# Kernel tuning notes

Measured on AMD Instinct MI355X. Metric: run time of the kernel, lower is better.

## Reference

```python
import jax, jax.numpy as jnp
import numpy as np

N = 4096
IN, HID, OUT = 512, 512, 512
EMB, MHID = 64, 128
GRID_SIZE, SPLINE_ORDER = 5, 3
D_B = GRID_SIZE + SPLINE_ORDER + 1      # 9
SPLINE_DIM = GRID_SIZE + SPLINE_ORDER   # 8


def make_grid():
    h = (1.0 - (-1.0)) / GRID_SIZE
    return jnp.arange(-SPLINE_ORDER, GRID_SIZE + SPLINE_ORDER + 1, dtype=jnp.float32) * h - 1.0


def b_splines(x, grid):
    # x: (N, in) -> (N, in, SPLINE_DIM); Cox-de Boor recursion, epsilon-stabilized
    xg = x[..., None]
    bases = ((xg >= grid[:-1]) & (xg < grid[1:])).astype(x.dtype)
    eps = 1e-08
    for k in range(1, SPLINE_ORDER + 1):
        dp = grid[k:-1] - grid[:-(k + 1)]
        dn = grid[k + 1:] - grid[1:-k]
        bases = (xg - grid[:-(k + 1)]) / (dp + eps) * bases[..., :-1] \
              + (grid[k + 1:] - xg) / (dn + eps) * bases[..., 1:]
    return bases


def _xavier(k, shape):
    fan_out, fan_in = shape
    std = (2.0 / (fan_in + fan_out)) ** 0.5
    return std * jax.random.normal(k, shape, jnp.float32)


def setup_inputs() -> dict:
    key = jax.random.key(0)
    ks = jax.random.split(key, 7)
    x = 2.0 * jax.random.uniform(ks[0], (N, IN), jnp.float32) - 1.0
    inp = {"x": x}
    dims = [(IN, HID), (HID, OUT)]
    for i, (fi, fo) in enumerate(dims):
        kk = jax.random.split(ks[i + 1], 3)
        inp[f"emb{i}"] = _xavier(kk[0], (fi * fo, EMB))   # layout: (out, in) flattened, out outer
        inp[f"w1_{i}"] = _xavier(kk[1], (MHID, EMB))
        inp[f"b1_{i}"] = jnp.zeros((MHID,), jnp.float32)
        inp[f"w2_{i}"] = _xavier(kk[2], (D_B, MHID))
        inp[f"b2_{i}"] = jnp.zeros((D_B,), jnp.float32)
    return inp


def _kan_layer(h, emb, w1, b1, w2, b2, in_f, out_f, grid):
    basis = b_splines(h, grid)                              # (N, in, SPLINE_DIM)
    w = (emb @ w1.T + b1) @ w2.T + b2                       # (out*in, D_B)
    w = w.reshape(out_f, in_f, D_B)
    w_spline = w[..., :SPLINE_DIM]                          # (out, in, SPLINE_DIM)
    w_base = w[..., SPLINE_DIM]                             # (out, in)  == weights[:, :, -1]
    out = jnp.einsum('nis,ois->no', basis, w_spline)
    out = out + jnp.einsum('ni,oi->no', jax.nn.silu(h), w_base)
    return out


def reference(x, emb0, w1_0, b1_0, w2_0, b2_0, emb1, w1_1, b1_1, w2_1, b2_1):
    grid = make_grid()
    h = _kan_layer(x, emb0, w1_0, b1_0, w2_0, b2_0, IN, HID, grid)
    h = _kan_layer(h, emb1, w1_1, b1_1, w2_1, b2_1, HID, OUT, grid)
    return h
```

## Files before the change

kernel.cpp:

```cpp
#include <hip/hip_runtime.h>
#include <cstdint>
#include <cstddef>

typedef unsigned short u16;
typedef unsigned int   u32;

typedef __bf16 bf16x8 __attribute__((ext_vector_type(8)));
typedef float  f32x4  __attribute__((ext_vector_type(4)));

#define NROWS 4096
#define INF   512
#define OUTF  512
#define EMB   64
#define MHID  128
#define DB    9
#define KDIM  (INF * DB)
#define MN    (NROWS * OUTF)

__device__ __forceinline__ u16 f2bf(float f) {
    union { float f; u32 ui; } v; v.f = f;
    u32 u = v.ui;
    u += 0x7fffu + ((u >> 16) & 1u);
    return (u16)(u >> 16);
}
__device__ __forceinline__ float gridv(int t) { return (float)(t - 3) * 0.4f - 1.0f; }

__global__ __launch_bounds__(256) void meff_kernel(
    const float* __restrict__ w1_0, const float* __restrict__ b1_0,
    const float* __restrict__ w2_0, const float* __restrict__ b2_0,
    const float* __restrict__ w1_1, const float* __restrict__ b1_1,
    const float* __restrict__ w2_1, const float* __restrict__ b2_1,
    float* __restrict__ Mc)
{
    int tid  = threadIdx.x;
    int lane = tid & 63;
    int wid  = blockIdx.x * 4 + (tid >> 6);
    if (wid >= 1170) return;
    int layer = wid / 585;
    int o     = wid % 585;
    const float* w1 = layer ? w1_1 : w1_0;
    const float* b1 = layer ? b1_1 : b1_0;
    const float* w2 = layer ? w2_1 : w2_0;
    const float* b2 = layer ? b2_1 : b2_0;

    float p;
    int d;
    if (o < 576) {
        int j = o / 9; d = o % 9;
        p = w1[lane * EMB + j]        * w2[d * MHID + lane]
          + w1[(lane + 64) * EMB + j] * w2[d * MHID + lane + 64];
    } else {
        d = o - 576;
        p = b1[lane] * w2[d * MHID + lane] + b1[lane + 64] * w2[d * MHID + lane + 64];
    }
#pragma unroll
    for (int off = 32; off >= 1; off >>= 1)
        p += __shfl_xor(p, off, 64);
    if (lane == 0) {
        if (o >= 576) p += b2[d];
        Mc[layer * 1024 + o] = p;
    }
}

__global__ __launch_bounds__(256) void genw_kernel(
    const float* __restrict__ emb0, const float* __restrict__ emb1,
    const float* __restrict__ Mc,
    u16* __restrict__ Bw0, u16* __restrict__ Bw1)
{
    __shared__ __align__(16) float4 tile[128 * 16];
    __shared__ __align__(16) float  pbuf[128 * 9];
    __shared__ __align__(16) u16    ob[128 * 9];
    int layer = blockIdx.y;
    const float* emb = layer ? emb1 : emb0;
    u16* Bw = layer ? Bw1 : Bw0;
    const float* mc = Mc + layer * 1024;

    int tid = threadIdx.x;
    size_t rowbase = (size_t)blockIdx.x * 128;

    const float4* g4 = (const float4*)(emb + rowbase * EMB);
#pragma unroll
    for (int q = 0; q < 8; ++q) {
        int f = q * 256 + tid;
        float4 v = g4[f];
        int row = f >> 4, c4 = f & 15;
        tile[row * 16 + (c4 ^ (row & 15))] = v;
    }
    __syncthreads();

    int r  = tid & 127;
    int hi = tid >> 7;
    int cb = hi * 8;
    const float* mcp = mc + __builtin_amdgcn_readfirstlane(hi) * 32 * 9;

    float acc[9];
#pragma unroll
    for (int d = 0; d < 9; ++d) acc[d] = hi ? 0.0f : mc[576 + d];

#pragma unroll
    for (int jj = 0; jj < 8; ++jj) {
        float4 v = tile[r * 16 + ((cb + jj) ^ (r & 15))];
#pragma unroll
        for (int d = 0; d < 9; ++d)
            acc[d] += v.x * mcp[(jj * 4 + 0) * 9 + d]
                    + v.y * mcp[(jj * 4 + 1) * 9 + d]
                    + v.z * mcp[(jj * 4 + 2) * 9 + d]
                    + v.w * mcp[(jj * 4 + 3) * 9 + d];
    }

    if (hi) {
#pragma unroll
        for (int d = 0; d < 9; ++d) pbuf[r * 9 + d] = acc[d];
    }
    __syncthreads();
    if (!hi) {
#pragma unroll
        for (int d = 0; d < 9; ++d) ob[r * 9 + d] = f2bf(acc[d] + pbuf[r * 9 + d]);
    }
    __syncthreads();

    const uint4* src = (const uint4*)ob;
    uint4* dst = (uint4*)(Bw + rowbase * 9);
    if (tid < 144) dst[tid] = src[tid];
}

__global__ __launch_bounds__(256) void phi_kernel(const float* __restrict__ xin,
                                                  const float* __restrict__ part,
                                                  int S,
                                                  u16* __restrict__ phi)
{
    __shared__ __align__(16) u16 lbuf[256 * 9];
    int tid = threadIdx.x;
    int idx = blockIdx.x * 256 + tid;

    float xv;
    if (part) {
        xv = 0.f;
        for (int z = 0; z < S; ++z) xv += part[(size_t)z * MN + idx];
    } else {
        xv = xin[idx];
    }

    float b[11];
#pragma unroll
    for (int t = 0; t < 11; ++t)
        b[t] = (xv >= gridv(t) && xv < gridv(t + 1)) ? 1.0f : 0.0f;
#pragma unroll
    for (int k = 1; k <= 3; ++k) {
#pragma unroll
        for (int t = 0; t + k < 11; ++t) {
            float rdp = 1.0f / ((gridv(t + k) - gridv(t)) + 1e-8f);
            float rdn = 1.0f / ((gridv(t + k + 1) - gridv(t + 1)) + 1e-8f);
            b[t] = (xv - gridv(t)) * rdp * b[t] + (gridv(t + k + 1) - xv) * rdn * b[t + 1];
        }
    }
    float sil = xv / (1.0f + expf(-xv));

#pragma unroll
    for (int d = 0; d < 8; ++d) lbuf[tid * 9 + d] = f2bf(b[d]);
    lbuf[tid * 9 + 8] = f2bf(sil);
    __syncthreads();

    const uint4* src = (const uint4*)lbuf;
    uint4* dst = (uint4*)(phi + (size_t)blockIdx.x * 256 * 9);
    for (int s = tid; s < 288; s += 256) dst[s] = src[s];
}

#define GLOAD16(gp, lp) __builtin_amdgcn_global_load_lds(                         \
    (const __attribute__((address_space(1))) u32*)(gp),                           \
    (__attribute__((address_space(3))) u32*)(lp), 16, 0, 0)

__global__ __launch_bounds__(256, 4) void gemm_kernel(const __bf16* __restrict__ A,
                                                      const __bf16* __restrict__ B,
                                                      float* __restrict__ Cpart,
                                                      int N, int K, int ksz)
{
    __shared__ __align__(16) __bf16 As[128 * 64];
    __shared__ __align__(16) __bf16 Bs[128 * 64];

    int tid  = threadIdx.x;
    int lane = tid & 63;
    int wv   = tid >> 6;
    int wm   = wv >> 1, wn = wv & 1;
    int brow = blockIdx.x * 128;
    int bcol = blockIdx.y * 128;
    int z    = blockIdx.z;
    int kbeg = z * ksz, kend = kbeg + ksz;

    f32x4 acc[4][4];
#pragma unroll
    for (int r = 0; r < 4; ++r)
#pragma unroll
        for (int c = 0; c < 4; ++c)
#pragma unroll
            for (int g = 0; g < 4; ++g) acc[r][c][g] = 0.0f;

    int quad = lane >> 4;
    int l16  = lane & 15;

    for (int k0 = kbeg; k0 < kend; k0 += 64) {
#pragma unroll
        for (int q = 0; q < 4; ++q) {
            int chunk = q * 256 + wv * 64 + lane;
            int row   = chunk >> 3;
            int slot  = chunk & 7;
            int col   = ((slot ^ (row & 7)) << 3);
            const __bf16* ga = A + (size_t)(brow + row) * K + (k0 + col);
            const __bf16* gb = B + (size_t)(bcol + row) * K + (k0 + col);
            GLOAD16(ga, &As[(q * 256 + wv * 64) * 8]);
            GLOAD16(gb, &Bs[(q * 256 + wv * 64) * 8]);
        }
        __syncthreads();

#pragma unroll
        for (int ks = 0; ks < 2; ++ks) {
            bf16x8 af[4], bfr[4];
#pragma unroll
            for (int r = 0; r < 4; ++r) {
                int arow = wm * 64 + r * 16 + l16;
                af[r] = *(const bf16x8*)&As[arow * 64 + (((ks * 4 + quad) ^ (arow & 7)) << 3)];
                int brw = wn * 64 + r * 16 + l16;
                bfr[r] = *(const bf16x8*)&Bs[brw * 64 + (((ks * 4 + quad) ^ (brw & 7)) << 3)];
            }
#pragma unroll
            for (int r = 0; r < 4; ++r)
#pragma unroll
                for (int c = 0; c < 4; ++c)
                    acc[r][c] = __builtin_amdgcn_mfma_f32_16x16x32_bf16(af[r], bfr[c], acc[r][c], 0, 0, 0);
        }
        __syncthreads();
    }

    float* Cz = Cpart + (size_t)z * MN;
#pragma unroll
    for (int r = 0; r < 4; ++r)
#pragma unroll
        for (int c = 0; c < 4; ++c)
#pragma unroll
            for (int g = 0; g < 4; ++g) {
                int grow = brow + wm * 64 + r * 16 + quad * 4 + g;
                int gcol = bcol + wn * 64 + c * 16 + l16;
                Cz[(size_t)grow * N + gcol] = acc[r][c][g];
            }
}

__global__ __launch_bounds__(256) void reduce_kernel(const float* __restrict__ part,
                                                     int S, float* __restrict__ out)
{
    int i = blockIdx.x * 256 + threadIdx.x;
    const float4* p4 = (const float4*)part;
    float4 s = p4[i];
    for (int z = 1; z < S; ++z) {
        float4 v = p4[(size_t)z * (MN / 4) + i];
        s.x += v.x; s.y += v.y; s.z += v.z; s.w += v.w;
    }
    ((float4*)out)[i] = s;
}

extern "C" void kernel_launch(void* const* d_in, const int* in_sizes, int n_in,
                              void* d_out, int out_size, void* d_ws, size_t ws_size,
                              hipStream_t stream)
{
    const float* x    = (const float*)d_in[0];
    const float* emb0 = (const float*)d_in[1];
    const float* w1_0 = (const float*)d_in[2];
    const float* b1_0 = (const float*)d_in[3];
    const float* w2_0 = (const float*)d_in[4];
    const float* b2_0 = (const float*)d_in[5];
    const float* emb1 = (const float*)d_in[6];
    const float* w1_1 = (const float*)d_in[7];
    const float* b1_1 = (const float*)d_in[8];
    const float* w2_1 = (const float*)d_in[9];
    const float* b2_1 = (const float*)d_in[10];

    char* ws = (char*)d_ws;
    const size_t PHI_OFF  = 0;
    const size_t BW0_OFF  = 37748736;
    const size_t BW1_OFF  = BW0_OFF + 4718592;
    const size_t MC_OFF   = BW1_OFF + 4718592;
    const size_t PART_OFF = MC_OFF + 8192;

    int S = 1;
    const size_t SLAB = 8388608ull;
    if      (ws_size >= PART_OFF + 4 * SLAB) S = 4;
    else if (ws_size >= PART_OFF + 2 * SLAB) S = 2;
    int ksz = KDIM / S;

    u16*   phi  = (u16*)(ws + PHI_OFF);
    u16*   Bw0  = (u16*)(ws + BW0_OFF);
    u16*   Bw1  = (u16*)(ws + BW1_OFF);
    float* Mc   = (float*)(ws + MC_OFF);
    float* part = (float*)(ws + PART_OFF);

    meff_kernel<<<293, 256, 0, stream>>>(w1_0, b1_0, w2_0, b2_0,
                                         w1_1, b1_1, w2_1, b2_1, Mc);
    genw_kernel<<<dim3(2048, 2), 256, 0, stream>>>(emb0, emb1, Mc, Bw0, Bw1);

    phi_kernel<<<8192, 256, 0, stream>>>(x, nullptr, 0, phi);
    gemm_kernel<<<dim3(32, 4, S), 256, 0, stream>>>((const __bf16*)phi, (const __bf16*)Bw0,
                                                    part, OUTF, KDIM, ksz);
    phi_kernel<<<8192, 256, 0, stream>>>(nullptr, part, S, phi);
    gemm_kernel<<<dim3(32, 4, S), 256, 0, stream>>>((const __bf16*)phi, (const __bf16*)Bw1,
                                                    part, OUTF, KDIM, ksz);
    reduce_kernel<<<2048, 256, 0, stream>>>(part, S, (float*)d_out);
}
```

Baseline: 260.9 us.

## Make genw kernel persistent with double-buffered async global-to-LDS loads

The weight-generation kernel now launches 256 blocks per layer instead of 2048, and each block handles 8 row chunks in a loop. The next chunk of embedding rows is prefetched with global_load_lds into a second LDS buffer while the current chunk is computed. The swizzle moves from the LDS write address to the global read address, so each lane can issue a direct 16-byte async copy. The goal is to hide the memory latency of this bandwidth-heavy stage, at the cost of fewer resident waves, double the tile LDS, and reliance on barriers to order the async LDS writes.

```diff
diff --git a/kernel.cpp b/kernel.cpp
--- a/kernel.cpp
+++ b/kernel.cpp
@@ -24,6 +24,10 @@
     return (u16)(u >> 16);
 }
 __device__ __forceinline__ float gridv(int t) { return (float)(t - 3) * 0.4f - 1.0f; }
+
+#define GLOAD16(gp, lp) __builtin_amdgcn_global_load_lds(                         \
+    (const __attribute__((address_space(1))) u32*)(gp),                           \
+    (__attribute__((address_space(3))) u32*)(lp), 16, 0, 0)
 
 __global__ __launch_bounds__(256) void meff_kernel(
     const float* __restrict__ w1_0, const float* __restrict__ b1_0,
@@ -62,12 +66,12 @@
     }
 }
 
-__global__ __launch_bounds__(256) void genw_kernel(
+__global__ __launch_bounds__(256, 2) void genw_kernel(
     const float* __restrict__ emb0, const float* __restrict__ emb1,
     const float* __restrict__ Mc,
     u16* __restrict__ Bw0, u16* __restrict__ Bw1)
 {
-    __shared__ __align__(16) float4 tile[128 * 16];
+    __shared__ __align__(16) float4 tile[2][128 * 16];
     __shared__ __align__(16) float  pbuf[128 * 9];
     __shared__ __align__(16) u16    ob[128 * 9];
     int layer = blockIdx.y;
@@ -76,52 +80,66 @@
     const float* mc = Mc + layer * 1024;
 
     int tid = threadIdx.x;
-    size_t rowbase = (size_t)blockIdx.x * 128;
-
-    const float4* g4 = (const float4*)(emb + rowbase * EMB);
-#pragma unroll
-    for (int q = 0; q < 8; ++q) {
-        int f = q * 256 + tid;
-        float4 v = g4[f];
-        int row = f >> 4, c4 = f & 15;
-        tile[row * 16 + (c4 ^ (row & 15))] = v;
-    }
+    int wb  = tid & ~63;
+    int r   = tid & 127;
+    int hi  = tid >> 7;
+    int cb  = hi * 8;
+    const float* mcp = mc + __builtin_amdgcn_readfirstlane(hi) * 32 * 9;
+
+    const int CH = 8;
+
+#define STAGE_GL(b, ch)                                                        \
+    {                                                                          \
+        const float4* g4 = (const float4*)(emb + (size_t)((ch) * 256 + blockIdx.x) * 128 * EMB); \
+        _Pragma("unroll")                                                      \
+        for (int q = 0; q < 8; ++q) {                                          \
+            int f   = q * 256 + tid;                                           \
+            int row = f >> 4, c4s = f & 15;                                    \
+            GLOAD16(g4 + row * 16 + (c4s ^ (row & 15)), &tile[b][q * 256 + wb]); \
+        }                                                                      \
+    }
+
+    STAGE_GL(0, 0);
     __syncthreads();
 
-    int r  = tid & 127;
-    int hi = tid >> 7;
-    int cb = hi * 8;
-    const float* mcp = mc + __builtin_amdgcn_readfirstlane(hi) * 32 * 9;
-
-    float acc[9];
-#pragma unroll
-    for (int d = 0; d < 9; ++d) acc[d] = hi ? 0.0f : mc[576 + d];
-
-#pragma unroll
-    for (int jj = 0; jj < 8; ++jj) {
-        float4 v = tile[r * 16 + ((cb + jj) ^ (r & 15))];
-#pragma unroll
-        for (int d = 0; d < 9; ++d)
-            acc[d] += v.x * mcp[(jj * 4 + 0) * 9 + d]
-                    + v.y * mcp[(jj * 4 + 1) * 9 + d]
-                    + v.z * mcp[(jj * 4 + 2) * 9 + d]
-                    + v.w * mcp[(jj * 4 + 3) * 9 + d];
-    }
-
-    if (hi) {
-#pragma unroll
-        for (int d = 0; d < 9; ++d) pbuf[r * 9 + d] = acc[d];
-    }
-    __syncthreads();
-    if (!hi) {
-#pragma unroll
-        for (int d = 0; d < 9; ++d) ob[r * 9 + d] = f2bf(acc[d] + pbuf[r * 9 + d]);
-    }
-    __syncthreads();
-
-    const uint4* src = (const uint4*)ob;
-    uint4* dst = (uint4*)(Bw + rowbase * 9);
-    if (tid < 144) dst[tid] = src[tid];
+    int cur = 0;
+    for (int ch = 0; ch < CH; ++ch) {
+        size_t rowbase = (size_t)(ch * 256 + blockIdx.x) * 128;
+
+        if (ch + 1 < CH) STAGE_GL(cur ^ 1, ch + 1);
+
+        float acc[9];
+#pragma unroll
+        for (int d = 0; d < 9; ++d) acc[d] = hi ? 0.0f : mc[576 + d];
+
+#pragma unroll
+        for (int jj = 0; jj < 8; ++jj) {
+            float4 v = tile[cur][r * 16 + ((cb + jj) ^ (r & 15))];
+#pragma unroll
+            for (int d = 0; d < 9; ++d)
+                acc[d] += v.x * mcp[(jj * 4 + 0) * 9 + d]
+                        + v.y * mcp[(jj * 4 + 1) * 9 + d]
+                        + v.z * mcp[(jj * 4 + 2) * 9 + d]
+                        + v.w * mcp[(jj * 4 + 3) * 9 + d];
+        }
+
+        if (hi) {
+#pragma unroll
+            for (int d = 0; d < 9; ++d) pbuf[r * 9 + d] = acc[d];
+        }
+        __syncthreads();
+        if (!hi) {
+#pragma unroll
+            for (int d = 0; d < 9; ++d) ob[r * 9 + d] = f2bf(acc[d] + pbuf[r * 9 + d]);
+        }
+        __syncthreads();
+
+        const uint4* src = (const uint4*)ob;
+        uint4* dst = (uint4*)(Bw + rowbase * 9);
+        if (tid < 144) dst[tid] = src[tid];
+        cur ^= 1;
+    }
+#undef STAGE_GL
 }
 
 __global__ __launch_bounds__(256) void phi_kernel(const float* __restrict__ xin,
@@ -165,10 +183,6 @@
     uint4* dst = (uint4*)(phi + (size_t)blockIdx.x * 256 * 9);
     for (int s = tid; s < 288; s += 256) dst[s] = src[s];
 }
-
-#define GLOAD16(gp, lp) __builtin_amdgcn_global_load_lds(                         \
-    (const __attribute__((address_space(1))) u32*)(gp),                           \
-    (__attribute__((address_space(3))) u32*)(lp), 16, 0, 0)
 
 __global__ __launch_bounds__(256, 4) void gemm_kernel(const __bf16* __restrict__ A,
                                                       const __bf16* __restrict__ B,
@@ -294,7 +308,7 @@
 
     meff_kernel<<<293, 256, 0, stream>>>(w1_0, b1_0, w2_0, b2_0,
                                          w1_1, b1_1, w2_1, b2_1, Mc);
-    genw_kernel<<<dim3(2048, 2), 256, 0, stream>>>(emb0, emb1, Mc, Bw0, Bw1);
+    genw_kernel<<<dim3(256, 2), 256, 0, stream>>>(emb0, emb1, Mc, Bw0, Bw1);
 
     phi_kernel<<<8192, 256, 0, stream>>>(x, nullptr, 0, phi);
     gemm_kernel<<<dim3(32, 4, S), 256, 0, stream>>>((const __bf16*)phi, (const __bf16*)Bw0,
```

Result: slower. 267.5 us (+2.5%).
